# Kernel tuning notes

Measured on AMD Instinct MI355X. Metric: run time of the kernel, lower is better.

Reference implementation:

```python
import jax, jax.numpy as jnp
import numpy as np

N = 16384      # number of PF candidates (nodes)
D_IN = 13      # pfc_input_dim
H = 16         # hidden_dim
K = 8          # kNN neighbors (includes self, dist 0, matching PyG knn(x, x, k))


def setup_inputs() -> dict:
    key = jax.random.key(0)
    ks = jax.random.split(key, 8)

    def w(k, shape):
        return (jax.random.normal(k, shape, dtype=jnp.float32) * 0.1)

    z = lambda n: jnp.zeros((n,), dtype=jnp.float32)
    return {
        "x_pfc": jax.random.normal(ks[0], (N, D_IN), dtype=jnp.float32),
        # pfc_encode: Linear(13,8) SiLU, Linear(8,16) SiLU, Linear(16,15)
        "W1": w(ks[1], (D_IN, H // 2)), "b1": z(H // 2),
        "W2": w(ks[2], (H // 2, H)),    "b2": z(H),
        "W3": w(ks[3], (H, H - 1)),     "b3": z(H - 1),
        # DynamicEdgeConv edge MLP: Linear(2H, H) SiLU
        "We": w(ks[4], (2 * H, H)),     "be": z(H),
        # ffn: Linear(H, 2H) SiLU, Linear(2H, H)
        "Wf1": w(ks[5], (H, 2 * H)),    "bf1": z(2 * H),
        "Wf2": w(ks[6], (2 * H, H)),    "bf2": z(H),
    }


def reference(x_pfc, W1, b1, W2, b2, W3, b3, We, be, Wf1, bf1, Wf2, bf2):
    silu = jax.nn.silu
    # pfc_encode (dropout = identity in eval)
    h = silu(x_pfc @ W1 + b1)
    h = silu(h @ W2 + b2)
    h = h @ W3 + b3                                   # [N, H-1]
    x = jnp.concatenate([h, x_pfc[:, -1:]], axis=1)   # [N, H]

    # Dynamic kNN graph in encoded-feature space (self included, dist 0)
    sq = jnp.sum(x * x, axis=1)                       # [N]
    d2 = sq[:, None] + sq[None, :] - 2.0 * (x @ x.T)  # [N, N] pairwise sq dist
    _, idx = jax.lax.top_k(-d2, K)                    # [N, K] neighbor indices

    # EdgeConv message: nn(cat([x_i, x_j - x_i])), mean aggregation
    x_j = x[idx]                                      # [N, K, H] gather
    x_i = x[:, None, :]                               # [N, 1, H]
    edge_in = jnp.concatenate(
        [jnp.broadcast_to(x_i, x_j.shape), x_j - x_i], axis=-1)  # [N, K, 2H]
    msg = silu(edge_in @ We + be)                     # [N, K, H]
    feats = jnp.mean(msg, axis=1)                     # [N, H]

    # ffn (dropout = identity in eval)
    f = silu(feats @ Wf1 + bf1)
    f = f @ Wf2 + bf2                                 # [N, H]
    return jnp.concatenate([f, x_pfc], axis=1)        # [N, H + D_IN]
```

## Files before the change

kernel.cpp:

```cpp
#include <hip/hip_runtime.h>
#include <math.h>

#define NPTS 16384
#define DIN 13
#define KNN 8
#define GL 12
#define BIGF 1.7014118e38f

typedef _Float16 half8 __attribute__((ext_vector_type(8)));
typedef float f32x4 __attribute__((ext_vector_type(4)));
typedef float f32x16 __attribute__((ext_vector_type(16)));

union HU4 { uint4 u; half8 h; };
union C16 { f32x16 w; f32x4 q[4]; };

__device__ __forceinline__ float silu(float v) {
    return v / (1.0f + __expf(-v));
}

#define MED3(v, a, b) __builtin_amdgcn_fmed3f((v), (a), (b))

#define INS8V(v) {                      \
    d7 = MED3((v), d6, d7);             \
    d6 = MED3((v), d5, d6);             \
    d5 = MED3((v), d4, d5);             \
    d4 = MED3((v), d3, d4);             \
    d3 = MED3((v), d2, d3);             \
    d2 = MED3((v), d1, d2);             \
    d1 = MED3((v), d0, d1);             \
    d0 = fminf((v), d0); }

#define INS12L(G, v) {                  \
    G##11 = MED3((v), G##10, G##11);    \
    G##10 = MED3((v), G##9, G##10);     \
    G##9  = MED3((v), G##8, G##9);      \
    G##8  = MED3((v), G##7, G##8);      \
    G##7  = MED3((v), G##6, G##7);      \
    G##6  = MED3((v), G##5, G##6);      \
    G##5  = MED3((v), G##4, G##5);      \
    G##4  = MED3((v), G##3, G##4);      \
    G##3  = MED3((v), G##2, G##3);      \
    G##2  = MED3((v), G##1, G##2);      \
    G##1  = MED3((v), G##0, G##1);      \
    G##0  = fminf((v), G##0); }

#define INS12G(v) INS12L(g, v)

#define CSW(p, q) { float lo_ = fminf(m##p, m##q); float hi_ = fmaxf(m##p, m##q); m##p = lo_; m##q = hi_; }

#define CLEAN16() \
    CSW(0,8) CSW(1,9) CSW(2,10) CSW(3,11) CSW(4,12) CSW(5,13) CSW(6,14) CSW(7,15) \
    CSW(0,4) CSW(1,5) CSW(2,6) CSW(3,7) CSW(8,12) CSW(9,13) CSW(10,14) CSW(11,15) \
    CSW(0,2) CSW(1,3) CSW(4,6) CSW(5,7) CSW(8,10) CSW(9,11) CSW(12,14) CSW(13,15) \
    CSW(0,1) CSW(2,3) CSW(4,5) CSW(6,7) CSW(8,9) CSW(10,11) CSW(12,13) CSW(14,15)

#define MERGE12_SHFLG(G, mask) {                              \
    float b0 = __shfl_xor(G##0, (mask), 64);                  \
    float b1 = __shfl_xor(G##1, (mask), 64);                  \
    float b2 = __shfl_xor(G##2, (mask), 64);                  \
    float b3 = __shfl_xor(G##3, (mask), 64);                  \
    float b4 = __shfl_xor(G##4, (mask), 64);                  \
    float b5 = __shfl_xor(G##5, (mask), 64);                  \
    float b6 = __shfl_xor(G##6, (mask), 64);                  \
    float b7 = __shfl_xor(G##7, (mask), 64);                  \
    float b8 = __shfl_xor(G##8, (mask), 64);                  \
    float b9 = __shfl_xor(G##9, (mask), 64);                  \
    float b10 = __shfl_xor(G##10, (mask), 64);                \
    float b11 = __shfl_xor(G##11, (mask), 64);                \
    float m0 = G##0, m1 = G##1, m2 = G##2, m3 = G##3;         \
    float m4 = fminf(G##4, b11), m5 = fminf(G##5, b10);       \
    float m6 = fminf(G##6, b9),  m7 = fminf(G##7, b8);        \
    float m8 = fminf(G##8, b7),  m9 = fminf(G##9, b6);        \
    float m10 = fminf(G##10, b5), m11 = fminf(G##11, b4);     \
    float m12 = b3, m13 = b2, m14 = b1, m15 = b0;             \
    CLEAN16();                                                \
    G##0 = m0; G##1 = m1; G##2 = m2; G##3 = m3;               \
    G##4 = m4; G##5 = m5; G##6 = m6; G##7 = m7;               \
    G##8 = m8; G##9 = m9; G##10 = m10; G##11 = m11; }

#define MERGE12_SHFL(mask) MERGE12_SHFLG(g, mask)

#define MERGE12_LDSG(G, LD) {                                 \
    float b0 = LD(0), b1 = LD(1), b2 = LD(2), b3 = LD(3);     \
    float b4 = LD(4), b5 = LD(5), b6 = LD(6), b7 = LD(7);     \
    float b8 = LD(8), b9 = LD(9), b10 = LD(10), b11 = LD(11); \
    float m0 = G##0, m1 = G##1, m2 = G##2, m3 = G##3;         \
    float m4 = fminf(G##4, b11), m5 = fminf(G##5, b10);       \
    float m6 = fminf(G##6, b9),  m7 = fminf(G##7, b8);        \
    float m8 = fminf(G##8, b7),  m9 = fminf(G##9, b6);        \
    float m10 = fminf(G##10, b5), m11 = fminf(G##11, b4);     \
    float m12 = b3, m13 = b2, m14 = b1, m15 = b0;             \
    CLEAN16();                                                \
    G##0 = m0; G##1 = m1; G##2 = m2; G##3 = m3;               \
    G##4 = m4; G##5 = m5; G##6 = m6; G##7 = m7;               \
    G##8 = m8; G##9 = m9; G##10 = m10; G##11 = m11; }

#define MERGE12_LDS(LD) MERGE12_LDSG(g, LD)

#define MERGE8(mask) {                                   \
    float b0 = __shfl_xor(d0, (mask), 64);               \
    float b1 = __shfl_xor(d1, (mask), 64);               \
    float b2 = __shfl_xor(d2, (mask), 64);               \
    float b3 = __shfl_xor(d3, (mask), 64);               \
    float b4 = __shfl_xor(d4, (mask), 64);               \
    float b5 = __shfl_xor(d5, (mask), 64);               \
    float b6 = __shfl_xor(d6, (mask), 64);               \
    float b7 = __shfl_xor(d7, (mask), 64);               \
    float m0 = fminf(d0, b7), m1 = fminf(d1, b6);        \
    float m2 = fminf(d2, b5), m3 = fminf(d3, b4);        \
    float m4 = fminf(d4, b3), m5 = fminf(d5, b2);        \
    float m6 = fminf(d6, b1), m7 = fminf(d7, b0);        \
    CSW(0,4) CSW(1,5) CSW(2,6) CSW(3,7)                  \
    CSW(0,2) CSW(1,3) CSW(4,6) CSW(5,7)                  \
    CSW(0,1) CSW(2,3) CSW(4,5) CSW(6,7)                  \
    d0 = m0; d1 = m1; d2 = m2; d3 = m3;                  \
    d4 = m4; d5 = m5; d6 = m6; d7 = m7; }

__global__ __launch_bounds__(64) void k_encoder(
    const float* __restrict__ x_pfc,
    const float* __restrict__ W1, const float* __restrict__ b1,
    const float* __restrict__ W2, const float* __restrict__ b2,
    const float* __restrict__ W3, const float* __restrict__ b3,
    const float* __restrict__ We, const float* __restrict__ be,
    float* __restrict__ xo, _Float16* __restrict__ H, _Float16* __restrict__ L,
    _Float16* __restrict__ YH, _Float16* __restrict__ YL,
    float* __restrict__ SQF, unsigned* __restrict__ SQHL,
    float* __restrict__ ACC)
{
    __shared__ float sW1[DIN * 8];
    __shared__ float sb1[8];
    __shared__ float sW2[8 * 16];
    __shared__ float sb2[16];
    __shared__ float sW3[16 * 15];
    __shared__ float sb3[15];
    __shared__ float sWe[16 * 16];
    __shared__ float sbe[16];
    int t = threadIdx.x;
    for (int q = t; q < DIN * 8; q += 64) sW1[q] = W1[q];
    for (int q = t; q < 8; q += 64) sb1[q] = b1[q];
    for (int q = t; q < 8 * 16; q += 64) sW2[q] = W2[q];
    for (int q = t; q < 16; q += 64) sb2[q] = b2[q];
    for (int q = t; q < 16 * 15; q += 64) sW3[q] = W3[q];
    for (int q = t; q < 15; q += 64) sb3[q] = b3[q];
    for (int q = t; q < 16 * 16; q += 64) sWe[q] = We[q];
    for (int q = t; q < 16; q += 64) sbe[q] = be[q];
    __syncthreads();

    int i = blockIdx.x * 64 + t;
    float in[DIN];
#pragma unroll
    for (int d = 0; d < DIN; ++d) in[d] = x_pfc[i * DIN + d];

    float a1[8];
#pragma unroll
    for (int h = 0; h < 8; ++h) a1[h] = sb1[h];
#pragma unroll
    for (int d = 0; d < DIN; ++d) {
        float v = in[d];
#pragma unroll
        for (int h = 0; h < 8; ++h) a1[h] += v * sW1[d * 8 + h];
    }
#pragma unroll
    for (int h = 0; h < 8; ++h) a1[h] = silu(a1[h]);

    float a2[16];
#pragma unroll
    for (int h = 0; h < 16; ++h) a2[h] = sb2[h];
#pragma unroll
    for (int d = 0; d < 8; ++d) {
        float v = a1[d];
#pragma unroll
        for (int h = 0; h < 16; ++h) a2[h] += v * sW2[d * 16 + h];
    }
#pragma unroll
    for (int h = 0; h < 16; ++h) a2[h] = silu(a2[h]);

    float a3[15];
#pragma unroll
    for (int h = 0; h < 15; ++h) a3[h] = sb3[h];
#pragma unroll
    for (int d = 0; d < 16; ++d) {
        float v = a2[d];
#pragma unroll
        for (int h = 0; h < 15; ++h) a3[h] += v * sW3[d * 15 + h];
    }

    float xr[16];
#pragma unroll
    for (int h = 0; h < 15; ++h) xr[h] = a3[h];
    xr[15] = in[DIN - 1];

    float s = 0.0f;
#pragma unroll
    for (int d = 0; d < 16; ++d) s += xr[d] * xr[d];

    float accb[16];
#pragma unroll
    for (int h = 0; h < 16; ++h) accb[h] = sbe[h];
#pragma unroll
    for (int d = 0; d < 16; ++d) {
        float v = xr[d];
#pragma unroll
        for (int h = 0; h < 16; ++h) accb[h] += v * sWe[d * 16 + h];
    }

    _Float16 hb[16], lb[16], yhb[16], ylb[16];
#pragma unroll
    for (int d = 0; d < 16; ++d) {
        _Float16 h = (_Float16)xr[d];
        hb[d] = h;
        lb[d] = (_Float16)(xr[d] - (float)h);
        float y = -2.0f * xr[d];
        _Float16 yh = (_Float16)y;
        yhb[d] = yh;
        ylb[d] = (_Float16)(y - (float)yh);
    }
    {
        uint4* p;
        p = (uint4*)(H + (size_t)i * 16);  p[0] = ((uint4*)hb)[0];  p[1] = ((uint4*)hb)[1];
        p = (uint4*)(L + (size_t)i * 16);  p[0] = ((uint4*)lb)[0];  p[1] = ((uint4*)lb)[1];
        p = (uint4*)(YH + (size_t)i * 16); p[0] = ((uint4*)yhb)[0]; p[1] = ((uint4*)yhb)[1];
        p = (uint4*)(YL + (size_t)i * 16); p[0] = ((uint4*)ylb)[0]; p[1] = ((uint4*)ylb)[1];
        f32x4* xq = (f32x4*)(xo + (size_t)i * 16);
        f32x4* aq = (f32x4*)(ACC + (size_t)i * 16);
#pragma unroll
        for (int q = 0; q < 4; ++q) {
            f32x4 xv, av;
#pragma unroll
            for (int r = 0; r < 4; ++r) { xv[r] = xr[q * 4 + r]; av[r] = accb[q * 4 + r]; }
            xq[q] = xv;
            aq[q] = av;
        }
    }
    SQF[i] = s;
    {
        _Float16 sh = (_Float16)s;
        _Float16 sl = (_Float16)(s - (float)sh);
        unsigned uh = *(const unsigned short*)&sh;
        unsigned ul = *(const unsigned short*)&sl;
        SQHL[i] = (ul << 16) | uh;
    }
}

__global__ __launch_bounds__(512, 4) void k_knn(
    const _Float16* __restrict__ H, const _Float16* __restrict__ L,
    const _Float16* __restrict__ YH, const _Float16* __restrict__ YL,
    const float* __restrict__ SQF, unsigned* __restrict__ CV)
{
    __shared__ float sBuf[8192];

    int t = threadIdx.x;
    int w = t >> 6;
    int lane = t & 63;
    int r31 = lane & 31;
    int hh = lane >> 5;
    int ih = blockIdx.x >> 1;
    int jh = blockIdx.x & 1;
    int i0 = ih * 64;

    int giA = i0 + r31;
    int giB = i0 + 32 + r31;
    half8 B1A = *(const half8*)(YH + (size_t)giA * 16 + hh * 8);
    half8 B2A = *(const half8*)(YL + (size_t)giA * 16 + hh * 8);
    half8 B1B = *(const half8*)(YH + (size_t)giB * 16 + hh * 8);
    half8 B2B = *(const half8*)(YL + (size_t)giB * 16 + hh * 8);

    {
        const f32x4* src = (const f32x4*)(SQF + jh * 8192);
        f32x4* dst = (f32x4*)sBuf;
        for (int q = t; q < 2048; q += 512) dst[q] = src[q];
    }

    float gA0 = BIGF, gA1 = BIGF, gA2 = BIGF, gA3 = BIGF;
    float gA4 = BIGF, gA5 = BIGF, gA6 = BIGF, gA7 = BIGF;
    float gA8 = BIGF, gA9 = BIGF, gA10 = BIGF, gA11 = BIGF;
    float gB0 = BIGF, gB1 = BIGF, gB2 = BIGF, gB3 = BIGF;
    float gB4 = BIGF, gB5 = BIGF, gB6 = BIGF, gB7 = BIGF;
    float gB8 = BIGF, gB9 = BIGF, gB10 = BIGF, gB11 = BIGF;

    int jw = jh * 8192 + w * 1024;
    const _Float16* pH = H + ((size_t)(jw + r31)) * 16 + hh * 8;
    const _Float16* pL = L + ((size_t)(jw + r31)) * 16 + hh * 8;
    const float* sqb = sBuf + w * 1024 + hh * 4;
    unsigned idt = (unsigned)((w << 1) | hh);

    __syncthreads();

#pragma unroll 2
    for (int tt = 0; tt < 32; ++tt) {
        half8 Ah = *(const half8*)(pH + (size_t)tt * 512);
        half8 Al = *(const half8*)(pL + (size_t)tt * 512);
        const f32x4* s_ = (const f32x4*)(sqb + tt * 32);
        f32x4 s0 = s_[0], s1 = s_[2], s2 = s_[4], s3 = s_[6];

        C16 cA, cB;
        cA.q[0] = s0; cA.q[1] = s1; cA.q[2] = s2; cA.q[3] = s3;
        cB.q[0] = s0; cB.q[1] = s1; cB.q[2] = s2; cB.q[3] = s3;
        cA.w = __builtin_amdgcn_mfma_f32_32x32x16_f16(Ah, B1A, cA.w, 0, 0, 0);
        cB.w = __builtin_amdgcn_mfma_f32_32x32x16_f16(Ah, B1B, cB.w, 0, 0, 0);
        cA.w = __builtin_amdgcn_mfma_f32_32x32x16_f16(Al, B1A, cA.w, 0, 0, 0);
        cB.w = __builtin_amdgcn_mfma_f32_32x32x16_f16(Al, B1B, cB.w, 0, 0, 0);
        cA.w = __builtin_amdgcn_mfma_f32_32x32x16_f16(Ah, B2A, cA.w, 0, 0, 0);
        cB.w = __builtin_amdgcn_mfma_f32_32x32x16_f16(Ah, B2B, cB.w, 0, 0, 0);

        unsigned idc = idt + (unsigned)(tt << 4);
        {
            float v0 = fminf(fminf(cA.w[0], cA.w[1]), cA.w[2]);
            float v1 = fminf(fminf(cA.w[3], cA.w[4]), cA.w[5]);
            float v2 = fminf(fminf(cA.w[6], cA.w[7]), cA.w[8]);
            float v3 = fminf(fminf(cA.w[9], cA.w[10]), cA.w[11]);
            float v4 = fminf(fminf(cA.w[12], cA.w[13]), cA.w[14]);
            float v5 = fminf(fminf(v0, v1), cA.w[15]);
            float v6 = fminf(fminf(v2, v3), v4);
            float vmin = fminf(v5, v6);
            unsigned pk = (__float_as_uint(vmin) & 0xFFFFFC00u) | idc;
            float pf = __uint_as_float(pk);
            INS12L(gA, pf);
        }
        {
            float v0 = fminf(fminf(cB.w[0], cB.w[1]), cB.w[2]);
            float v1 = fminf(fminf(cB.w[3], cB.w[4]), cB.w[5]);
            float v2 = fminf(fminf(cB.w[6], cB.w[7]), cB.w[8]);
            float v3 = fminf(fminf(cB.w[9], cB.w[10]), cB.w[11]);
            float v4 = fminf(fminf(cB.w[12], cB.w[13]), cB.w[14]);
            float v5 = fminf(fminf(v0, v1), cB.w[15]);
            float v6 = fminf(fminf(v2, v3), v4);
            float vmin = fminf(v5, v6);
            unsigned pk = (__float_as_uint(vmin) & 0xFFFFFC00u) | idc;
            float pf = __uint_as_float(pk);
            INS12L(gB, pf);
        }
    }

    MERGE12_SHFLG(gA, 32);
    MERGE12_SHFLG(gB, 32);

    __syncthreads();

#define STORE24() if (lane < 32) {                         \
        sBuf[(w * 24 + 0) * 32 + r31] = gA0;               \
        sBuf[(w * 24 + 1) * 32 + r31] = gA1;               \
        sBuf[(w * 24 + 2) * 32 + r31] = gA2;               \
        sBuf[(w * 24 + 3) * 32 + r31] = gA3;               \
        sBuf[(w * 24 + 4) * 32 + r31] = gA4;               \
        sBuf[(w * 24 + 5) * 32 + r31] = gA5;               \
        sBuf[(w * 24 + 6) * 32 + r31] = gA6;               \
        sBuf[(w * 24 + 7) * 32 + r31] = gA7;               \
        sBuf[(w * 24 + 8) * 32 + r31] = gA8;               \
        sBuf[(w * 24 + 9) * 32 + r31] = gA9;               \
        sBuf[(w * 24 + 10) * 32 + r31] = gA10;             \
        sBuf[(w * 24 + 11) * 32 + r31] = gA11;             \
        sBuf[(w * 24 + 12) * 32 + r31] = gB0;              \
        sBuf[(w * 24 + 13) * 32 + r31] = gB1;              \
        sBuf[(w * 24 + 14) * 32 + r31] = gB2;              \
        sBuf[(w * 24 + 15) * 32 + r31] = gB3;              \
        sBuf[(w * 24 + 16) * 32 + r31] = gB4;              \
        sBuf[(w * 24 + 17) * 32 + r31] = gB5;              \
        sBuf[(w * 24 + 18) * 32 + r31] = gB6;              \
        sBuf[(w * 24 + 19) * 32 + r31] = gB7;              \
        sBuf[(w * 24 + 20) * 32 + r31] = gB8;              \
        sBuf[(w * 24 + 21) * 32 + r31] = gB9;              \
        sBuf[(w * 24 + 22) * 32 + r31] = gB10;             \
        sBuf[(w * 24 + 23) * 32 + r31] = gB11; }

#define MERGE_STEP(pw) {                                   \
        int pw_ = (pw);                                    \
        const float* mb = sBuf + (pw_ * 24) * 32 + r31;    \
        { _Pragma("clang diagnostic push")                 \
          ; }                                              \
        {                                                  \
        }                                                  \
    }

    if (w >= 4) STORE24();
    __syncthreads();
    if (w < 4) {
        int pw = w + 4;
#define LDA(s) sBuf[(pw * 24 + (s)) * 32 + r31]
#define LDB(s) sBuf[(pw * 24 + 12 + (s)) * 32 + r31]
        MERGE12_LDSG(gA, LDA);
        MERGE12_LDSG(gB, LDB);
#undef LDA
#undef LDB
    }
    __syncthreads();
    if (w == 2 || w == 3) STORE24();
    __syncthreads();
    if (w < 2) {
        int pw = w + 2;
#define LDA(s) sBuf[(pw * 24 + (s)) * 32 + r31]
#define LDB(s) sBuf[(pw * 24 + 12 + (s)) * 32 + r31]
        MERGE12_LDSG(gA, LDA);
        MERGE12_LDSG(gB, LDB);
#undef LDA
#undef LDB
    }
    __syncthreads();
    if (w == 1) STORE24();
    __syncthreads();
    if (w == 0) {
        int pw = 1;
#define LDA(s) sBuf[(pw * 24 + (s)) * 32 + r31]
#define LDB(s) sBuf[(pw * 24 + 12 + (s)) * 32 + r31]
        MERGE12_LDSG(gA, LDA);
        MERGE12_LDSG(gB, LDB);
#undef LDA
#undef LDB
        if (lane < 32) {
            unsigned jb = ((unsigned)jh) << 9;
            size_t baseA = ((size_t)jh * NPTS + (i0 + r31)) * GL;
            size_t baseB = ((size_t)jh * NPTS + (i0 + 32 + r31)) * GL;
            CV[baseA + 0] = __float_as_uint(gA0) | jb;
            CV[baseA + 1] = __float_as_uint(gA1) | jb;
            CV[baseA + 2] = __float_as_uint(gA2) | jb;
            CV[baseA + 3] = __float_as_uint(gA3) | jb;
            CV[baseA + 4] = __float_as_uint(gA4) | jb;
            CV[baseA + 5] = __float_as_uint(gA5) | jb;
            CV[baseA + 6] = __float_as_uint(gA6) | jb;
            CV[baseA + 7] = __float_as_uint(gA7) | jb;
            CV[baseA + 8] = __float_as_uint(gA8) | jb;
            CV[baseA + 9] = __float_as_uint(gA9) | jb;
            CV[baseA + 10] = __float_as_uint(gA10) | jb;
            CV[baseA + 11] = __float_as_uint(gA11) | jb;
            CV[baseB + 0] = __float_as_uint(gB0) | jb;
            CV[baseB + 1] = __float_as_uint(gB1) | jb;
            CV[baseB + 2] = __float_as_uint(gB2) | jb;
            CV[baseB + 3] = __float_as_uint(gB3) | jb;
            CV[baseB + 4] = __float_as_uint(gB4) | jb;
            CV[baseB + 5] = __float_as_uint(gB5) | jb;
            CV[baseB + 6] = __float_as_uint(gB6) | jb;
            CV[baseB + 7] = __float_as_uint(gB7) | jb;
            CV[baseB + 8] = __float_as_uint(gB8) | jb;
            CV[baseB + 9] = __float_as_uint(gB9) | jb;
            CV[baseB + 10] = __float_as_uint(gB10) | jb;
            CV[baseB + 11] = __float_as_uint(gB11) | jb;
        }
    }
#undef STORE24
#undef MERGE_STEP
}

__global__ __launch_bounds__(512, 4) void k_head(
    const float* __restrict__ x, const unsigned* __restrict__ CV,
    const float* __restrict__ SQF,
    const float* __restrict__ x_pfc, const float* __restrict__ ACC,
    const float* __restrict__ We,
    const float* __restrict__ Wf1, const float* __restrict__ bf1,
    const float* __restrict__ Wf2, const float* __restrict__ bf2,
    float* __restrict__ out)
{
    __shared__ float sWe2[16 * 16];
    __shared__ float sWf1[16 * 32];
    __shared__ float sbf1[32];
    __shared__ float sWf2[32 * 16];
    __shared__ float sbf2[16];
    __shared__ int sGrp[32][GL];
    __shared__ int cnt[32];
    __shared__ int sIdx[32 * 8];
    __shared__ float sF1[32 * 33];
    int t = threadIdx.x;
    for (int q = t; q < 16 * 16; q += 512) sWe2[q] = We[256 + q];
    for (int q = t; q < 16 * 32; q += 512) sWf1[q] = Wf1[q];
    for (int q = t; q < 32; q += 512) sbf1[q] = bf1[q];
    for (int q = t; q < 32 * 16; q += 512) sWf2[q] = Wf2[q];
    for (int q = t; q < 16; q += 512) sbf2[q] = bf2[q];

    int i0 = blockIdx.x * 32;

    if (t < 64) {
        int pi = t & 31;
        int hf = t >> 5;
        const f32x4* c = (const f32x4*)(CV + ((size_t)hf * NPTS + (i0 + pi)) * GL);
        f32x4 c0 = c[0], c1 = c[1], c2 = c[2];
        float g0 = c0[0], g1 = c0[1], g2 = c0[2], g3 = c0[3];
        float g4 = c1[0], g5 = c1[1], g6 = c1[2], g7 = c1[3];
        float g8 = c2[0], g9 = c2[1], g10 = c2[2], g11 = c2[3];
        MERGE12_SHFL(32);
        if (t < 32) {
            cnt[pi] = 0;
#define DECJB(gk, s) { unsigned id_ = __float_as_uint(gk) & 0x3FFu;          \
            sGrp[pi][s] = (int)(((id_ >> 9) & 1) * 8192 + ((id_ >> 1) & 7) * 1024 + \
                                ((id_ >> 4) & 31) * 32 + (id_ & 1) * 4); }
            DECJB(g0, 0) DECJB(g1, 1) DECJB(g2, 2) DECJB(g3, 3)
            DECJB(g4, 4) DECJB(g5, 5) DECJB(g6, 6) DECJB(g7, 7)
            DECJB(g8, 8) DECJB(g9, 9) DECJB(g10, 10) DECJB(g11, 11)
#undef DECJB
        }
    }
    __syncthreads();

    int l = t & 15;
    int pt = t >> 4;
    int ql = l & 3;
    int qd = l >> 2;
    int i = i0 + pt;

    float xi[16];
    {
        const f32x4* xiv = (const f32x4*)(x + (size_t)i * 16);
#pragma unroll
        for (int q = 0; q < 4; ++q) {
            f32x4 a = xiv[q];
#pragma unroll
            for (int r = 0; r < 4; ++r) xi[q * 4 + r] = a[r];
        }
    }
    f32x4 xiq = ((const f32x4*)(x + (size_t)i * 16))[ql];

    float val[12];
    float d0 = BIGF, d1 = BIGF, d2 = BIGF, d3 = BIGF;
    float d4 = BIGF, d5 = BIGF, d6 = BIGF, d7 = BIGF;
#pragma unroll
    for (int g = 0; g < GL; ++g) {
        int jb = sGrp[pt][g];
        float vg = BIGF;
#pragma unroll
        for (int rho = 0; rho < 4; ++rho) {
            f32x4 a = *((const f32x4*)(x + ((size_t)(jb + rho * 8)) * 16) + l);
            float qdot = xiq[0] * a[0];
            qdot = fmaf(xiq[1], a[1], qdot);
            qdot = fmaf(xiq[2], a[2], qdot);
            qdot = fmaf(xiq[3], a[3], qdot);
            qdot += __shfl_xor(qdot, 1, 64);
            qdot += __shfl_xor(qdot, 2, 64);
            float v = fmaf(qdot, -2.0f, SQF[jb + rho * 8 + qd]);
            vg = (ql == rho) ? v : vg;
        }
        val[g] = vg;
        INS8V(vg);
    }

    MERGE8(1);
    MERGE8(2);
    MERGE8(4);
    MERGE8(8);
    float kth = d7;

#pragma unroll
    for (int g = 0; g < GL; ++g) {
        float v = val[g];
        if (v <= kth) {
            int j = sGrp[pt][g] + ql * 8 + qd;
            int p = atomicAdd(&cnt[pt], 1);
            if (p < KNN) sIdx[pt * 8 + p] = j;
        }
    }
    __syncthreads();

    int e8 = l & 7;
    int j = sIdx[pt * 8 + e8];

    float xd[16];
    {
        const f32x4* xjv = (const f32x4*)(x + (size_t)j * 16);
#pragma unroll
        for (int q = 0; q < 4; ++q) {
            f32x4 a = xjv[q];
#pragma unroll
            for (int r = 0; r < 4; ++r) xd[q * 4 + r] = a[r] - xi[q * 4 + r];
        }
    }

    float acc[16];
    {
        const f32x4* av = (const f32x4*)(ACC + (size_t)i * 16);
#pragma unroll
        for (int q = 0; q < 4; ++q) {
            f32x4 a = av[q];
#pragma unroll
            for (int r = 0; r < 4; ++r) acc[q * 4 + r] = a[r];
        }
    }
#pragma unroll
    for (int d = 0; d < 16; ++d) {
        float v = xd[d];
#pragma unroll
        for (int h = 0; h < 16; ++h) acc[h] += v * sWe2[d * 16 + h];
    }

    float feats[16];
#pragma unroll
    for (int h = 0; h < 16; ++h) feats[h] = silu(acc[h]);

#pragma unroll
    for (int mask = 1; mask <= 4; mask <<= 1) {
#pragma unroll
        for (int h = 0; h < 16; ++h) feats[h] += __shfl_xor(feats[h], mask, 64);
    }
#pragma unroll
    for (int h = 0; h < 16; ++h) feats[h] *= 0.125f;

    float p0 = sbf1[l];
    float p1 = sbf1[l + 16];
#pragma unroll
    for (int k = 0; k < 16; ++k) {
        float v = feats[k];
        p0 = fmaf(v, sWf1[k * 32 + l], p0);
        p1 = fmaf(v, sWf1[k * 32 + l + 16], p1);
    }
    p0 = silu(p0);
    p1 = silu(p1);
    sF1[pt * 33 + l] = p0;
    sF1[pt * 33 + 16 + l] = p1;
    __syncthreads();

    float o = sbf2[l];
#pragma unroll
    for (int k = 0; k < 32; ++k)
        o = fmaf(sF1[pt * 33 + k], sWf2[k * 16 + l], o);

    out[(size_t)i * 29 + l] = o;
    if (l < DIN) out[(size_t)i * 29 + 16 + l] = x_pfc[i * DIN + l];
}

extern "C" void kernel_launch(void* const* d_in, const int* in_sizes, int n_in,
                              void* d_out, int out_size, void* d_ws, size_t ws_size,
                              hipStream_t stream)
{
    const float* x_pfc = (const float*)d_in[0];
    const float* W1 = (const float*)d_in[1];
    const float* b1 = (const float*)d_in[2];
    const float* W2 = (const float*)d_in[3];
    const float* b2 = (const float*)d_in[4];
    const float* W3 = (const float*)d_in[5];
    const float* b3 = (const float*)d_in[6];
    const float* We = (const float*)d_in[7];
    const float* be = (const float*)d_in[8];
    const float* Wf1 = (const float*)d_in[9];
    const float* bf1 = (const float*)d_in[10];
    const float* Wf2 = (const float*)d_in[11];
    const float* bf2 = (const float*)d_in[12];
    float* out = (float*)d_out;

    float* xw = (float*)d_ws;
    float* ACCa = xw + (size_t)NPTS * 16;
    _Float16* Ha = (_Float16*)(ACCa + (size_t)NPTS * 16);
    _Float16* La = Ha + (size_t)NPTS * 16;
    _Float16* YHa = La + (size_t)NPTS * 16;
    _Float16* YLa = YHa + (size_t)NPTS * 16;
    float* SQFa = (float*)(YLa + (size_t)NPTS * 16);
    unsigned* SQHLa = (unsigned*)(SQFa + NPTS);
    unsigned* CVa = SQHLa + NPTS;

    hipLaunchKernelGGL(k_encoder, dim3(NPTS / 64), dim3(64), 0, stream,
                       x_pfc, W1, b1, W2, b2, W3, b3, We, be,
                       xw, Ha, La, YHa, YLa, SQFa, SQHLa, ACCa);
    hipLaunchKernelGGL(k_knn, dim3(NPTS / 64 * 2), dim3(512), 0, stream,
                       Ha, La, YHa, YLa, SQFa, CVa);
    hipLaunchKernelGGL(k_head, dim3(NPTS / 32), dim3(512), 0, stream,
                       xw, CVa, SQFa, x_pfc, ACCa, We, Wf1, bf1, Wf2, bf2, out);
}
```

Baseline: 150.3 us.

## Fuse kNN candidate search and head into one kernel over full column range

Merges the kNN scan and the head kernel into a single kernel. Each 512-thread block now scans all 16384 columns for 64 query rows instead of half the columns per block, so the cross-half candidate merge through global memory and the extra kernel launch go away. The candidate list stays in shared memory, and shared memory is reused through a union between the scan stage and the head stage. The cost is half as many blocks (256 on a large GPU), a 64KB shared buffer that may limit occupancy, and the head stage now running in two serial passes inside the block.

```diff
diff --git a/kernel.cpp b/kernel.cpp
--- a/kernel.cpp
+++ b/kernel.cpp
@@ -11,7 +11,6 @@
 typedef float f32x4 __attribute__((ext_vector_type(4)));
 typedef float f32x16 __attribute__((ext_vector_type(16)));
 
-union HU4 { uint4 u; half8 h; };
 union C16 { f32x16 w; f32x4 q[4]; };
 
 __device__ __forceinline__ float silu(float v) {
@@ -43,8 +42,6 @@
     G##2  = MED3((v), G##1, G##2);      \
     G##1  = MED3((v), G##0, G##1);      \
     G##0  = fminf((v), G##0); }
-
-#define INS12G(v) INS12L(g, v)
 
 #define CSW(p, q) { float lo_ = fminf(m##p, m##q); float hi_ = fmaxf(m##p, m##q); m##p = lo_; m##q = hi_; }
 
@@ -78,8 +75,6 @@
     G##4 = m4; G##5 = m5; G##6 = m6; G##7 = m7;               \
     G##8 = m8; G##9 = m9; G##10 = m10; G##11 = m11; }
 
-#define MERGE12_SHFL(mask) MERGE12_SHFLG(g, mask)
-
 #define MERGE12_LDSG(G, LD) {                                 \
     float b0 = LD(0), b1 = LD(1), b2 = LD(2), b3 = LD(3);     \
     float b4 = LD(4), b5 = LD(5), b6 = LD(6), b7 = LD(7);     \
@@ -94,8 +89,6 @@
     G##0 = m0; G##1 = m1; G##2 = m2; G##3 = m3;               \
     G##4 = m4; G##5 = m5; G##6 = m6; G##7 = m7;               \
     G##8 = m8; G##9 = m9; G##10 = m10; G##11 = m11; }
-
-#define MERGE12_LDS(LD) MERGE12_LDSG(g, LD)
 
 #define MERGE8(mask) {                                   \
     float b0 = __shfl_xor(d0, (mask), 64);               \
@@ -124,8 +117,7 @@
     const float* __restrict__ We, const float* __restrict__ be,
     float* __restrict__ xo, _Float16* __restrict__ H, _Float16* __restrict__ L,
     _Float16* __restrict__ YH, _Float16* __restrict__ YL,
-    float* __restrict__ SQF, unsigned* __restrict__ SQHL,
-    float* __restrict__ ACC)
+    float* __restrict__ SQF, float* __restrict__ ACC)
 {
     __shared__ float sW1[DIN * 8];
     __shared__ float sb1[8];
@@ -233,384 +225,348 @@
         }
     }
     SQF[i] = s;
-    {
-        _Float16 sh = (_Float16)s;
-        _Float16 sl = (_Float16)(s - (float)sh);
-        unsigned uh = *(const unsigned short*)&sh;
-        unsigned ul = *(const unsigned short*)&sl;
-        SQHL[i] = (ul << 16) | uh;
-    }
 }
 
-__global__ __launch_bounds__(512, 4) void k_knn(
+__global__ __launch_bounds__(512, 4) void k_knn_head(
     const _Float16* __restrict__ H, const _Float16* __restrict__ L,
     const _Float16* __restrict__ YH, const _Float16* __restrict__ YL,
-    const float* __restrict__ SQF, unsigned* __restrict__ CV)
-{
-    __shared__ float sBuf[8192];
-
-    int t = threadIdx.x;
-    int w = t >> 6;
-    int lane = t & 63;
-    int r31 = lane & 31;
-    int hh = lane >> 5;
-    int ih = blockIdx.x >> 1;
-    int jh = blockIdx.x & 1;
-    int i0 = ih * 64;
-
-    int giA = i0 + r31;
-    int giB = i0 + 32 + r31;
-    half8 B1A = *(const half8*)(YH + (size_t)giA * 16 + hh * 8);
-    half8 B2A = *(const half8*)(YL + (size_t)giA * 16 + hh * 8);
-    half8 B1B = *(const half8*)(YH + (size_t)giB * 16 + hh * 8);
-    half8 B2B = *(const half8*)(YL + (size_t)giB * 16 + hh * 8);
-
-    {
-        const f32x4* src = (const f32x4*)(SQF + jh * 8192);
-        f32x4* dst = (f32x4*)sBuf;
-        for (int q = t; q < 2048; q += 512) dst[q] = src[q];
-    }
-
-    float gA0 = BIGF, gA1 = BIGF, gA2 = BIGF, gA3 = BIGF;
-    float gA4 = BIGF, gA5 = BIGF, gA6 = BIGF, gA7 = BIGF;
-    float gA8 = BIGF, gA9 = BIGF, gA10 = BIGF, gA11 = BIGF;
-    float gB0 = BIGF, gB1 = BIGF, gB2 = BIGF, gB3 = BIGF;
-    float gB4 = BIGF, gB5 = BIGF, gB6 = BIGF, gB7 = BIGF;
-    float gB8 = BIGF, gB9 = BIGF, gB10 = BIGF, gB11 = BIGF;
-
-    int jw = jh * 8192 + w * 1024;
-    const _Float16* pH = H + ((size_t)(jw + r31)) * 16 + hh * 8;
-    const _Float16* pL = L + ((size_t)(jw + r31)) * 16 + hh * 8;
-    const float* sqb = sBuf + w * 1024 + hh * 4;
-    unsigned idt = (unsigned)((w << 1) | hh);
-
-    __syncthreads();
-
-#pragma unroll 2
-    for (int tt = 0; tt < 32; ++tt) {
-        half8 Ah = *(const half8*)(pH + (size_t)tt * 512);
-        half8 Al = *(const half8*)(pL + (size_t)tt * 512);
-        const f32x4* s_ = (const f32x4*)(sqb + tt * 32);
-        f32x4 s0 = s_[0], s1 = s_[2], s2 = s_[4], s3 = s_[6];
-
-        C16 cA, cB;
-        cA.q[0] = s0; cA.q[1] = s1; cA.q[2] = s2; cA.q[3] = s3;
-        cB.q[0] = s0; cB.q[1] = s1; cB.q[2] = s2; cB.q[3] = s3;
-        cA.w = __builtin_amdgcn_mfma_f32_32x32x16_f16(Ah, B1A, cA.w, 0, 0, 0);
-        cB.w = __builtin_amdgcn_mfma_f32_32x32x16_f16(Ah, B1B, cB.w, 0, 0, 0);
-        cA.w = __builtin_amdgcn_mfma_f32_32x32x16_f16(Al, B1A, cA.w, 0, 0, 0);
-        cB.w = __builtin_amdgcn_mfma_f32_32x32x16_f16(Al, B1B, cB.w, 0, 0, 0);
-        cA.w = __builtin_amdgcn_mfma_f32_32x32x16_f16(Ah, B2A, cA.w, 0, 0, 0);
-        cB.w = __builtin_amdgcn_mfma_f32_32x32x16_f16(Ah, B2B, cB.w, 0, 0, 0);
-
-        unsigned idc = idt + (unsigned)(tt << 4);
-        {
-            float v0 = fminf(fminf(cA.w[0], cA.w[1]), cA.w[2]);
-            float v1 = fminf(fminf(cA.w[3], cA.w[4]), cA.w[5]);
-            float v2 = fminf(fminf(cA.w[6], cA.w[7]), cA.w[8]);
-            float v3 = fminf(fminf(cA.w[9], cA.w[10]), cA.w[11]);
-            float v4 = fminf(fminf(cA.w[12], cA.w[13]), cA.w[14]);
-            float v5 = fminf(fminf(v0, v1), cA.w[15]);
-            float v6 = fminf(fminf(v2, v3), v4);
-            float vmin = fminf(v5, v6);
-            unsigned pk = (__float_as_uint(vmin) & 0xFFFFFC00u) | idc;
-            float pf = __uint_as_float(pk);
-            INS12L(gA, pf);
-        }
-        {
-            float v0 = fminf(fminf(cB.w[0], cB.w[1]), cB.w[2]);
-            float v1 = fminf(fminf(cB.w[3], cB.w[4]), cB.w[5]);
-            float v2 = fminf(fminf(cB.w[6], cB.w[7]), cB.w[8]);
-            float v3 = fminf(fminf(cB.w[9], cB.w[10]), cB.w[11]);
-            float v4 = fminf(fminf(cB.w[12], cB.w[13]), cB.w[14]);
-            float v5 = fminf(fminf(v0, v1), cB.w[15]);
-            float v6 = fminf(fminf(v2, v3), v4);
-            float vmin = fminf(v5, v6);
-            unsigned pk = (__float_as_uint(vmin) & 0xFFFFFC00u) | idc;
-            float pf = __uint_as_float(pk);
-            INS12L(gB, pf);
-        }
-    }
-
-    MERGE12_SHFLG(gA, 32);
-    MERGE12_SHFLG(gB, 32);
-
-    __syncthreads();
-
-#define STORE24() if (lane < 32) {                         \
-        sBuf[(w * 24 + 0) * 32 + r31] = gA0;               \
-        sBuf[(w * 24 + 1) * 32 + r31] = gA1;               \
-        sBuf[(w * 24 + 2) * 32 + r31] = gA2;               \
-        sBuf[(w * 24 + 3) * 32 + r31] = gA3;               \
-        sBuf[(w * 24 + 4) * 32 + r31] = gA4;               \
-        sBuf[(w * 24 + 5) * 32 + r31] = gA5;               \
-        sBuf[(w * 24 + 6) * 32 + r31] = gA6;               \
-        sBuf[(w * 24 + 7) * 32 + r31] = gA7;               \
-        sBuf[(w * 24 + 8) * 32 + r31] = gA8;               \
-        sBuf[(w * 24 + 9) * 32 + r31] = gA9;               \
-        sBuf[(w * 24 + 10) * 32 + r31] = gA10;             \
-        sBuf[(w * 24 + 11) * 32 + r31] = gA11;             \
-        sBuf[(w * 24 + 12) * 32 + r31] = gB0;              \
-        sBuf[(w * 24 + 13) * 32 + r31] = gB1;              \
-        sBuf[(w * 24 + 14) * 32 + r31] = gB2;              \
-        sBuf[(w * 24 + 15) * 32 + r31] = gB3;              \
-        sBuf[(w * 24 + 16) * 32 + r31] = gB4;              \
-        sBuf[(w * 24 + 17) * 32 + r31] = gB5;              \
-        sBuf[(w * 24 + 18) * 32 + r31] = gB6;              \
-        sBuf[(w * 24 + 19) * 32 + r31] = gB7;              \
-        sBuf[(w * 24 + 20) * 32 + r31] = gB8;              \
-        sBuf[(w * 24 + 21) * 32 + r31] = gB9;              \
-        sBuf[(w * 24 + 22) * 32 + r31] = gB10;             \
-        sBuf[(w * 24 + 23) * 32 + r31] = gB11; }
-
-#define MERGE_STEP(pw) {                                   \
-        int pw_ = (pw);                                    \
-        const float* mb = sBuf + (pw_ * 24) * 32 + r31;    \
-        { _Pragma("clang diagnostic push")                 \
-          ; }                                              \
-        {                                                  \
-        }                                                  \
-    }
-
-    if (w >= 4) STORE24();
-    __syncthreads();
-    if (w < 4) {
-        int pw = w + 4;
-#define LDA(s) sBuf[(pw * 24 + (s)) * 32 + r31]
-#define LDB(s) sBuf[(pw * 24 + 12 + (s)) * 32 + r31]
-        MERGE12_LDSG(gA, LDA);
-        MERGE12_LDSG(gB, LDB);
-#undef LDA
-#undef LDB
-    }
-    __syncthreads();
-    if (w == 2 || w == 3) STORE24();
-    __syncthreads();
-    if (w < 2) {
-        int pw = w + 2;
-#define LDA(s) sBuf[(pw * 24 + (s)) * 32 + r31]
-#define LDB(s) sBuf[(pw * 24 + 12 + (s)) * 32 + r31]
-        MERGE12_LDSG(gA, LDA);
-        MERGE12_LDSG(gB, LDB);
-#undef LDA
-#undef LDB
-    }
-    __syncthreads();
-    if (w == 1) STORE24();
-    __syncthreads();
-    if (w == 0) {
-        int pw = 1;
-#define LDA(s) sBuf[(pw * 24 + (s)) * 32 + r31]
-#define LDB(s) sBuf[(pw * 24 + 12 + (s)) * 32 + r31]
-        MERGE12_LDSG(gA, LDA);
-        MERGE12_LDSG(gB, LDB);
-#undef LDA
-#undef LDB
-        if (lane < 32) {
-            unsigned jb = ((unsigned)jh) << 9;
-            size_t baseA = ((size_t)jh * NPTS + (i0 + r31)) * GL;
-            size_t baseB = ((size_t)jh * NPTS + (i0 + 32 + r31)) * GL;
-            CV[baseA + 0] = __float_as_uint(gA0) | jb;
-            CV[baseA + 1] = __float_as_uint(gA1) | jb;
-            CV[baseA + 2] = __float_as_uint(gA2) | jb;
-            CV[baseA + 3] = __float_as_uint(gA3) | jb;
-            CV[baseA + 4] = __float_as_uint(gA4) | jb;
-            CV[baseA + 5] = __float_as_uint(gA5) | jb;
-            CV[baseA + 6] = __float_as_uint(gA6) | jb;
-            CV[baseA + 7] = __float_as_uint(gA7) | jb;
-            CV[baseA + 8] = __float_as_uint(gA8) | jb;
-            CV[baseA + 9] = __float_as_uint(gA9) | jb;
-            CV[baseA + 10] = __float_as_uint(gA10) | jb;
-            CV[baseA + 11] = __float_as_uint(gA11) | jb;
-            CV[baseB + 0] = __float_as_uint(gB0) | jb;
-            CV[baseB + 1] = __float_as_uint(gB1) | jb;
-            CV[baseB + 2] = __float_as_uint(gB2) | jb;
-            CV[baseB + 3] = __float_as_uint(gB3) | jb;
-            CV[baseB + 4] = __float_as_uint(gB4) | jb;
-            CV[baseB + 5] = __float_as_uint(gB5) | jb;
-            CV[baseB + 6] = __float_as_uint(gB6) | jb;
-            CV[baseB + 7] = __float_as_uint(gB7) | jb;
-            CV[baseB + 8] = __float_as_uint(gB8) | jb;
-            CV[baseB + 9] = __float_as_uint(gB9) | jb;
-            CV[baseB + 10] = __float_as_uint(gB10) | jb;
-            CV[baseB + 11] = __float_as_uint(gB11) | jb;
-        }
-    }
-#undef STORE24
-#undef MERGE_STEP
-}
-
-__global__ __launch_bounds__(512, 4) void k_head(
-    const float* __restrict__ x, const unsigned* __restrict__ CV,
-    const float* __restrict__ SQF,
+    const float* __restrict__ SQF, const float* __restrict__ x,
     const float* __restrict__ x_pfc, const float* __restrict__ ACC,
     const float* __restrict__ We,
     const float* __restrict__ Wf1, const float* __restrict__ bf1,
     const float* __restrict__ Wf2, const float* __restrict__ bf2,
     float* __restrict__ out)
 {
-    __shared__ float sWe2[16 * 16];
-    __shared__ float sWf1[16 * 32];
-    __shared__ float sbf1[32];
-    __shared__ float sWf2[32 * 16];
-    __shared__ float sbf2[16];
-    __shared__ int sGrp[32][GL];
-    __shared__ int cnt[32];
-    __shared__ int sIdx[32 * 8];
-    __shared__ float sF1[32 * 33];
+    __shared__ union SU {
+        float knn[16384];
+        struct {
+            float we2[256]; float wf1[512]; float bf1s[32];
+            float wf2[512]; float bf2s[16];
+            int cnt[64]; int idx[64 * 8];
+            float f1[32 * 33];
+        } h;
+    } S;
+    __shared__ unsigned sList[64 * GL];
+
     int t = threadIdx.x;
-    for (int q = t; q < 16 * 16; q += 512) sWe2[q] = We[256 + q];
-    for (int q = t; q < 16 * 32; q += 512) sWf1[q] = Wf1[q];
-    for (int q = t; q < 32; q += 512) sbf1[q] = bf1[q];
-    for (int q = t; q < 32 * 16; q += 512) sWf2[q] = Wf2[q];
-    for (int q = t; q < 16; q += 512) sbf2[q] = bf2[q];
-
-    int i0 = blockIdx.x * 32;
-
-    if (t < 64) {
-        int pi = t & 31;
-        int hf = t >> 5;
-        const f32x4* c = (const f32x4*)(CV + ((size_t)hf * NPTS + (i0 + pi)) * GL);
-        f32x4 c0 = c[0], c1 = c[1], c2 = c[2];
-        float g0 = c0[0], g1 = c0[1], g2 = c0[2], g3 = c0[3];
-        float g4 = c1[0], g5 = c1[1], g6 = c1[2], g7 = c1[3];
-        float g8 = c2[0], g9 = c2[1], g10 = c2[2], g11 = c2[3];
-        MERGE12_SHFL(32);
-        if (t < 32) {
-            cnt[pi] = 0;
-#define DECJB(gk, s) { unsigned id_ = __float_as_uint(gk) & 0x3FFu;          \
-            sGrp[pi][s] = (int)(((id_ >> 9) & 1) * 8192 + ((id_ >> 1) & 7) * 1024 + \
-                                ((id_ >> 4) & 31) * 32 + (id_ & 1) * 4); }
-            DECJB(g0, 0) DECJB(g1, 1) DECJB(g2, 2) DECJB(g3, 3)
-            DECJB(g4, 4) DECJB(g5, 5) DECJB(g6, 6) DECJB(g7, 7)
-            DECJB(g8, 8) DECJB(g9, 9) DECJB(g10, 10) DECJB(g11, 11)
-#undef DECJB
+    int w = t >> 6;
+    int lane = t & 63;
+    int r31 = lane & 31;
+    int hh = lane >> 5;
+    int i0 = blockIdx.x * 64;
+
+    {
+        int giA = i0 + r31;
+        int giB = i0 + 32 + r31;
+        half8 B1A = *(const half8*)(YH + (size_t)giA * 16 + hh * 8);
+        half8 B2A = *(const half8*)(YL + (size_t)giA * 16 + hh * 8);
+        half8 B1B = *(const half8*)(YH + (size_t)giB * 16 + hh * 8);
+        half8 B2B = *(const half8*)(YL + (size_t)giB * 16 + hh * 8);
+
+        {
+            const f32x4* src = (const f32x4*)SQF;
+            f32x4* dst = (f32x4*)S.knn;
+            for (int q = t; q < 4096; q += 512) dst[q] = src[q];
         }
-    }
+
+        float gA0 = BIGF, gA1 = BIGF, gA2 = BIGF, gA3 = BIGF;
+        float gA4 = BIGF, gA5 = BIGF, gA6 = BIGF, gA7 = BIGF;
+        float gA8 = BIGF, gA9 = BIGF, gA10 = BIGF, gA11 = BIGF;
+        float gB0 = BIGF, gB1 = BIGF, gB2 = BIGF, gB3 = BIGF;
+        float gB4 = BIGF, gB5 = BIGF, gB6 = BIGF, gB7 = BIGF;
+        float gB8 = BIGF, gB9 = BIGF, gB10 = BIGF, gB11 = BIGF;
+
+        const _Float16* pH = H + ((size_t)(w * 2048 + r31)) * 16 + hh * 8;
+        const _Float16* pL = L + ((size_t)(w * 2048 + r31)) * 16 + hh * 8;
+        const float* sqb = S.knn + w * 2048 + hh * 4;
+        unsigned idt = (unsigned)((w << 1) | hh);
+
+        __syncthreads();
+
+#pragma unroll 2
+        for (int tt = 0; tt < 64; ++tt) {
+            half8 Ah = *(const half8*)(pH + (size_t)tt * 512);
+            half8 Al = *(const half8*)(pL + (size_t)tt * 512);
+            const f32x4* s_ = (const f32x4*)(sqb + tt * 32);
+            f32x4 s0 = s_[0], s1 = s_[2], s2 = s_[4], s3 = s_[6];
+
+            C16 cA, cB;
+            cA.q[0] = s0; cA.q[1] = s1; cA.q[2] = s2; cA.q[3] = s3;
+            cB.q[0] = s0; cB.q[1] = s1; cB.q[2] = s2; cB.q[3] = s3;
+            cA.w = __builtin_amdgcn_mfma_f32_32x32x16_f16(Ah, B1A, cA.w, 0, 0, 0);
+            cB.w = __builtin_amdgcn_mfma_f32_32x32x16_f16(Ah, B1B, cB.w, 0, 0, 0);
+            cA.w = __builtin_amdgcn_mfma_f32_32x32x16_f16(Al, B1A, cA.w, 0, 0, 0);
+            cB.w = __builtin_amdgcn_mfma_f32_32x32x16_f16(Al, B1B, cB.w, 0, 0, 0);
+            cA.w = __builtin_amdgcn_mfma_f32_32x32x16_f16(Ah, B2A, cA.w, 0, 0, 0);
+            cB.w = __builtin_amdgcn_mfma_f32_32x32x16_f16(Ah, B2B, cB.w, 0, 0, 0);
+
+            unsigned idc = idt + (unsigned)(tt << 4);
+            {
+                float v0 = fminf(fminf(cA.w[0], cA.w[1]), cA.w[2]);
+                float v1 = fminf(fminf(cA.w[3], cA.w[4]), cA.w[5]);
+                float v2 = fminf(fminf(cA.w[6], cA.w[7]), cA.w[8]);
+                float v3 = fminf(fminf(cA.w[9], cA.w[10]), cA.w[11]);
+                float v4 = fminf(fminf(cA.w[12], cA.w[13]), cA.w[14]);
+                float v5 = fminf(fminf(v0, v1), cA.w[15]);
+                float v6 = fminf(fminf(v2, v3), v4);
+                float vmin = fminf(v5, v6);
+                unsigned pk = (__float_as_uint(vmin) & 0xFFFFFC00u) | idc;
+                float pf = __uint_as_float(pk);
+                INS12L(gA, pf);
+            }
+            {
+                float v0 = fminf(fminf(cB.w[0], cB.w[1]), cB.w[2]);
+                float v1 = fminf(fminf(cB.w[3], cB.w[4]), cB.w[5]);
+                float v2 = fminf(fminf(cB.w[6], cB.w[7]), cB.w[8]);
+                float v3 = fminf(fminf(cB.w[9], cB.w[10]), cB.w[11]);
+                float v4 = fminf(fminf(cB.w[12], cB.w[13]), cB.w[14]);
+                float v5 = fminf(fminf(v0, v1), cB.w[15]);
+                float v6 = fminf(fminf(v2, v3), v4);
+                float vmin = fminf(v5, v6);
+                unsigned pk = (__float_as_uint(vmin) & 0xFFFFFC00u) | idc;
+                float pf = __uint_as_float(pk);
+                INS12L(gB, pf);
+            }
+        }
+
+        MERGE12_SHFLG(gA, 32);
+        MERGE12_SHFLG(gB, 32);
+
+        __syncthreads();
+
+#define STORE24() if (lane < 32) {                           \
+            S.knn[(w * 24 + 0) * 32 + r31] = gA0;            \
+            S.knn[(w * 24 + 1) * 32 + r31] = gA1;            \
+            S.knn[(w * 24 + 2) * 32 + r31] = gA2;            \
+            S.knn[(w * 24 + 3) * 32 + r31] = gA3;            \
+            S.knn[(w * 24 + 4) * 32 + r31] = gA4;            \
+            S.knn[(w * 24 + 5) * 32 + r31] = gA5;            \
+            S.knn[(w * 24 + 6) * 32 + r31] = gA6;            \
+            S.knn[(w * 24 + 7) * 32 + r31] = gA7;            \
+            S.knn[(w * 24 + 8) * 32 + r31] = gA8;            \
+            S.knn[(w * 24 + 9) * 32 + r31] = gA9;            \
+            S.knn[(w * 24 + 10) * 32 + r31] = gA10;          \
+            S.knn[(w * 24 + 11) * 32 + r31] = gA11;          \
+            S.knn[(w * 24 + 12) * 32 + r31] = gB0;           \
+            S.knn[(w * 24 + 13) * 32 + r31] = gB1;           \
+            S.knn[(w * 24 + 14) * 32 + r31] = gB2;           \
+            S.knn[(w * 24 + 15) * 32 + r31] = gB3;           \
+            S.knn[(w * 24 + 16) * 32 + r31] = gB4;           \
+            S.knn[(w * 24 + 17) * 32 + r31] = gB5;           \
+            S.knn[(w * 24 + 18) * 32 + r31] = gB6;           \
+            S.knn[(w * 24 + 19) * 32 + r31] = gB7;           \
+            S.knn[(w * 24 + 20) * 32 + r31] = gB8;           \
+            S.knn[(w * 24 + 21) * 32 + r31] = gB9;           \
+            S.knn[(w * 24 + 22) * 32 + r31] = gB10;          \
+            S.knn[(w * 24 + 23) * 32 + r31] = gB11; }
+
+        if (w >= 4) STORE24();
+        __syncthreads();
+        if (w < 4) {
+            int pw = w + 4;
+#define LDA(s) S.knn[(pw * 24 + (s)) * 32 + r31]
+#define LDB(s) S.knn[(pw * 24 + 12 + (s)) * 32 + r31]
+            MERGE12_LDSG(gA, LDA);
+            MERGE12_LDSG(gB, LDB);
+#undef LDA
+#undef LDB
+        }
+        __syncthreads();
+        if (w == 2 || w == 3) STORE24();
+        __syncthreads();
+        if (w < 2) {
+            int pw = w + 2;
+#define LDA(s) S.knn[(pw * 24 + (s)) * 32 + r31]
+#define LDB(s) S.knn[(pw * 24 + 12 + (s)) * 32 + r31]
+            MERGE12_LDSG(gA, LDA);
+            MERGE12_LDSG(gB, LDB);
+#undef LDA
+#undef LDB
+        }
+        __syncthreads();
+        if (w == 1) STORE24();
+        __syncthreads();
+        if (w == 0) {
+            int pw = 1;
+#define LDA(s) S.knn[(pw * 24 + (s)) * 32 + r31]
+#define LDB(s) S.knn[(pw * 24 + 12 + (s)) * 32 + r31]
+            MERGE12_LDSG(gA, LDA);
+            MERGE12_LDSG(gB, LDB);
+#undef LDA
+#undef LDB
+            if (lane < 32) {
+                sList[r31 * GL + 0] = __float_as_uint(gA0);
+                sList[r31 * GL + 1] = __float_as_uint(gA1);
+                sList[r31 * GL + 2] = __float_as_uint(gA2);
+                sList[r31 * GL + 3] = __float_as_uint(gA3);
+                sList[r31 * GL + 4] = __float_as_uint(gA4);
+                sList[r31 * GL + 5] = __float_as_uint(gA5);
+                sList[r31 * GL + 6] = __float_as_uint(gA6);
+                sList[r31 * GL + 7] = __float_as_uint(gA7);
+                sList[r31 * GL + 8] = __float_as_uint(gA8);
+                sList[r31 * GL + 9] = __float_as_uint(gA9);
+                sList[r31 * GL + 10] = __float_as_uint(gA10);
+                sList[r31 * GL + 11] = __float_as_uint(gA11);
+                sList[(32 + r31) * GL + 0] = __float_as_uint(gB0);
+                sList[(32 + r31) * GL + 1] = __float_as_uint(gB1);
+                sList[(32 + r31) * GL + 2] = __float_as_uint(gB2);
+                sList[(32 + r31) * GL + 3] = __float_as_uint(gB3);
+                sList[(32 + r31) * GL + 4] = __float_as_uint(gB4);
+                sList[(32 + r31) * GL + 5] = __float_as_uint(gB5);
+                sList[(32 + r31) * GL + 6] = __float_as_uint(gB6);
+                sList[(32 + r31) * GL + 7] = __float_as_uint(gB7);
+                sList[(32 + r31) * GL + 8] = __float_as_uint(gB8);
+                sList[(32 + r31) * GL + 9] = __float_as_uint(gB9);
+                sList[(32 + r31) * GL + 10] = __float_as_uint(gB10);
+                sList[(32 + r31) * GL + 11] = __float_as_uint(gB11);
+            }
+        }
+#undef STORE24
+    }
+
     __syncthreads();
 
-    int l = t & 15;
-    int pt = t >> 4;
-    int ql = l & 3;
-    int qd = l >> 2;
-    int i = i0 + pt;
-
-    float xi[16];
     {
-        const f32x4* xiv = (const f32x4*)(x + (size_t)i * 16);
-#pragma unroll
-        for (int q = 0; q < 4; ++q) {
-            f32x4 a = xiv[q];
-#pragma unroll
-            for (int r = 0; r < 4; ++r) xi[q * 4 + r] = a[r];
+        for (int q = t; q < 16 * 16; q += 512) S.h.we2[q] = We[256 + q];
+        for (int q = t; q < 16 * 32; q += 512) S.h.wf1[q] = Wf1[q];
+        for (int q = t; q < 32; q += 512) S.h.bf1s[q] = bf1[q];
+        for (int q = t; q < 32 * 16; q += 512) S.h.wf2[q] = Wf2[q];
+        for (int q = t; q < 16; q += 512) S.h.bf2s[q] = bf2[q];
+        if (t < 64) S.h.cnt[t] = 0;
+        __syncthreads();
+
+        int l = t & 15;
+        int ptl = t >> 4;
+        int ql = l & 3;
+        int qd = l >> 2;
+
+#pragma unroll 1
+        for (int pass = 0; pass < 2; ++pass) {
+            int pt = pass * 32 + ptl;
+            int i = i0 + pt;
+
+            float xi[16];
+            {
+                const f32x4* xiv = (const f32x4*)(x + (size_t)i * 16);
+#pragma unroll
+                for (int q = 0; q < 4; ++q) {
+                    f32x4 a = xiv[q];
+#pragma unroll
+                    for (int r = 0; r < 4; ++r) xi[q * 4 + r] = a[r];
+                }
+            }
+            f32x4 xiq = ((const f32x4*)(x + (size_t)i * 16))[ql];
+
+            float val[12];
+            int jbs[12];
+            float d0 = BIGF, d1 = BIGF, d2 = BIGF, d3 = BIGF;
+            float d4 = BIGF, d5 = BIGF, d6 = BIGF, d7 = BIGF;
+#pragma unroll
+            for (int g = 0; g < GL; ++g) {
+                unsigned id = sList[pt * GL + g] & 0x3FFu;
+                int jb = (int)(((id >> 1) & 7) * 2048 + (id >> 4) * 32 + (id & 1) * 4);
+                jbs[g] = jb;
+                float vg = BIGF;
+#pragma unroll
+                for (int rho = 0; rho < 4; ++rho) {
+                    f32x4 a = *((const f32x4*)(x + ((size_t)(jb + rho * 8)) * 16) + l);
+                    float qdot = xiq[0] * a[0];
+                    qdot = fmaf(xiq[1], a[1], qdot);
+                    qdot = fmaf(xiq[2], a[2], qdot);
+                    qdot = fmaf(xiq[3], a[3], qdot);
+                    qdot += __shfl_xor(qdot, 1, 64);
+                    qdot += __shfl_xor(qdot, 2, 64);
+                    float v = fmaf(qdot, -2.0f, SQF[jb + rho * 8 + qd]);
+                    vg = (ql == rho) ? v : vg;
+                }
+                val[g] = vg;
+                INS8V(vg);
+            }
+
+            MERGE8(1);
+            MERGE8(2);
+            MERGE8(4);
+            MERGE8(8);
+            float kth = d7;
+
+#pragma unroll
+            for (int g = 0; g < GL; ++g) {
+                float v = val[g];
+                if (v <= kth) {
+                    int j = jbs[g] + ql * 8 + qd;
+                    int p = atomicAdd(&S.h.cnt[pt], 1);
+                    if (p < KNN) S.h.idx[pt * 8 + p] = j;
+                }
+            }
+            __syncthreads();
+
+            int e8 = l & 7;
+            int j = S.h.idx[pt * 8 + e8];
+
+            float xd[16];
+            {
+                const f32x4* xjv = (const f32x4*)(x + (size_t)j * 16);
+#pragma unroll
+                for (int q = 0; q < 4; ++q) {
+                    f32x4 a = xjv[q];
+#pragma unroll
+                    for (int r = 0; r < 4; ++r) xd[q * 4 + r] = a[r] - xi[q * 4 + r];
+                }
+            }
+
+            float acc[16];
+            {
+                const f32x4* av = (const f32x4*)(ACC + (size_t)i * 16);
+#pragma unroll
+                for (int q = 0; q < 4; ++q) {
+                    f32x4 a = av[q];
+#pragma unroll
+                    for (int r = 0; r < 4; ++r) acc[q * 4 + r] = a[r];
+                }
+            }
+#pragma unroll
+            for (int d = 0; d < 16; ++d) {
+                float v = xd[d];
+#pragma unroll
+                for (int h = 0; h < 16; ++h) acc[h] += v * S.h.we2[d * 16 + h];
+            }
+
+            float feats[16];
+#pragma unroll
+            for (int h = 0; h < 16; ++h) feats[h] = silu(acc[h]);
+
+#pragma unroll
+            for (int mask = 1; mask <= 4; mask <<= 1) {
+#pragma unroll
+                for (int h = 0; h < 16; ++h) feats[h] += __shfl_xor(feats[h], mask, 64);
+            }
+#pragma unroll
+            for (int h = 0; h < 16; ++h) feats[h] *= 0.125f;
+
+            float p0 = S.h.bf1s[l];
+            float p1 = S.h.bf1s[l + 16];
+#pragma unroll
+            for (int k = 0; k < 16; ++k) {
+                float v = feats[k];
+                p0 = fmaf(v, S.h.wf1[k * 32 + l], p0);
+                p1 = fmaf(v, S.h.wf1[k * 32 + l + 16], p1);
+            }
+            p0 = silu(p0);
+            p1 = silu(p1);
+            S.h.f1[ptl * 33 + l] = p0;
+            S.h.f1[ptl * 33 + 16 + l] = p1;
+            __syncthreads();
+
+            float o = S.h.bf2s[l];
+#pragma unroll
+            for (int k = 0; k < 32; ++k)
+                o = fmaf(S.h.f1[ptl * 33 + k], S.h.wf2[k * 16 + l], o);
+
+            out[(size_t)i * 29 + l] = o;
+            if (l < DIN) out[(size_t)i * 29 + 16 + l] = x_pfc[i * DIN + l];
+            __syncthreads();
         }
     }
-    f32x4 xiq = ((const f32x4*)(x + (size_t)i * 16))[ql];
-
-    float val[12];
-    float d0 = BIGF, d1 = BIGF, d2 = BIGF, d3 = BIGF;
-    float d4 = BIGF, d5 = BIGF, d6 = BIGF, d7 = BIGF;
-#pragma unroll
-    for (int g = 0; g < GL; ++g) {
-        int jb = sGrp[pt][g];
-        float vg = BIGF;
-#pragma unroll
-        for (int rho = 0; rho < 4; ++rho) {
-            f32x4 a = *((const f32x4*)(x + ((size_t)(jb + rho * 8)) * 16) + l);
-            float qdot = xiq[0] * a[0];
-            qdot = fmaf(xiq[1], a[1], qdot);
-            qdot = fmaf(xiq[2], a[2], qdot);
-            qdot = fmaf(xiq[3], a[3], qdot);
-            qdot += __shfl_xor(qdot, 1, 64);
-            qdot += __shfl_xor(qdot, 2, 64);
-            float v = fmaf(qdot, -2.0f, SQF[jb + rho * 8 + qd]);
-            vg = (ql == rho) ? v : vg;
-        }
-        val[g] = vg;
-        INS8V(vg);
-    }
-
-    MERGE8(1);
-    MERGE8(2);
-    MERGE8(4);
-    MERGE8(8);
-    float kth = d7;
-
-#pragma unroll
-    for (int g = 0; g < GL; ++g) {
-        float v = val[g];
-        if (v <= kth) {
-            int j = sGrp[pt][g] + ql * 8 + qd;
-            int p = atomicAdd(&cnt[pt], 1);
-            if (p < KNN) sIdx[pt * 8 + p] = j;
-        }
-    }
-    __syncthreads();
-
-    int e8 = l & 7;
-    int j = sIdx[pt * 8 + e8];
-
-    float xd[16];
-    {
-        const f32x4* xjv = (const f32x4*)(x + (size_t)j * 16);
-#pragma unroll
-        for (int q = 0; q < 4; ++q) {
-            f32x4 a = xjv[q];
-#pragma unroll
-            for (int r = 0; r < 4; ++r) xd[q * 4 + r] = a[r] - xi[q * 4 + r];
-        }
-    }
-
-    float acc[16];
-    {
-        const f32x4* av = (const f32x4*)(ACC + (size_t)i * 16);
-#pragma unroll
-        for (int q = 0; q < 4; ++q) {
-            f32x4 a = av[q];
-#pragma unroll
-            for (int r = 0; r < 4; ++r) acc[q * 4 + r] = a[r];
-        }
-    }
-#pragma unroll
-    for (int d = 0; d < 16; ++d) {
-        float v = xd[d];
-#pragma unroll
-        for (int h = 0; h < 16; ++h) acc[h] += v * sWe2[d * 16 + h];
-    }
-
-    float feats[16];
-#pragma unroll
-    for (int h = 0; h < 16; ++h) feats[h] = silu(acc[h]);
-
-#pragma unroll
-    for (int mask = 1; mask <= 4; mask <<= 1) {
-#pragma unroll
-        for (int h = 0; h < 16; ++h) feats[h] += __shfl_xor(feats[h], mask, 64);
-    }
-#pragma unroll
-    for (int h = 0; h < 16; ++h) feats[h] *= 0.125f;
-
-    float p0 = sbf1[l];
-    float p1 = sbf1[l + 16];
-#pragma unroll
-    for (int k = 0; k < 16; ++k) {
-        float v = feats[k];
-        p0 = fmaf(v, sWf1[k * 32 + l], p0);
-        p1 = fmaf(v, sWf1[k * 32 + l + 16], p1);
-    }
-    p0 = silu(p0);
-    p1 = silu(p1);
-    sF1[pt * 33 + l] = p0;
-    sF1[pt * 33 + 16 + l] = p1;
-    __syncthreads();
-
-    float o = sbf2[l];
-#pragma unroll
-    for (int k = 0; k < 32; ++k)
-        o = fmaf(sF1[pt * 33 + k], sWf2[k * 16 + l], o);
-
-    out[(size_t)i * 29 + l] = o;
-    if (l < DIN) out[(size_t)i * 29 + 16 + l] = x_pfc[i * DIN + l];
 }
 
 extern "C" void kernel_launch(void* const* d_in, const int* in_sizes, int n_in,
@@ -639,14 +595,11 @@
     _Float16* YHa = La + (size_t)NPTS * 16;
     _Float16* YLa = YHa + (size_t)NPTS * 16;
     float* SQFa = (float*)(YLa + (size_t)NPTS * 16);
-    unsigned* SQHLa = (unsigned*)(SQFa + NPTS);
-    unsigned* CVa = SQHLa + NPTS;
 
     hipLaunchKernelGGL(k_encoder, dim3(NPTS / 64), dim3(64), 0, stream,
                        x_pfc, W1, b1, W2, b2, W3, b3, We, be,
-                       xw, Ha, La, YHa, YLa, SQFa, SQHLa, ACCa);
-    hipLaunchKernelGGL(k_knn, dim3(NPTS / 64 * 2), dim3(512), 0, stream,
-                       Ha, La, YHa, YLa, SQFa, CVa);
-    hipLaunchKernelGGL(k_head, dim3(NPTS / 32), dim3(512), 0, stream,
-                       xw, CVa, SQFa, x_pfc, ACCa, We, Wf1, bf1, Wf2, bf2, out);
+                       xw, Ha, La, YHa, YLa, SQFa, ACCa);
+    hipLaunchKernelGGL(k_knn_head, dim3(NPTS / 64), dim3(512), 0, stream,
+                       Ha, La, YHa, YLa, SQFa, xw, x_pfc, ACCa,
+                       We, Wf1, bf1, Wf2, bf2, out);
 }
```

New measurement: 139.6 us. 1.08x faster.
